# Kernel tuning notes

Measured on AMD Instinct MI355X. Metric: run time of the kernel, lower is better.

## Reference

```python
import jax, jax.numpy as jnp
import numpy as np

H = 8  # num_heads

def setup_inputs() -> dict:
    key = jax.random.key(0)
    ks = jax.random.split(key, 10)
    B, N, D, E = 1, 4096, 256, 65536
    s = 0.02
    return {
        "x": jax.random.normal(ks[0], (B, N, D), jnp.float32),
        "edge_index": jax.random.randint(ks[1], (2, E), 0, N, jnp.int32),
        "edge_attr": jax.random.normal(ks[2], (E, 3), jnp.float32),
        "Wq": jax.random.normal(ks[3], (D, D), jnp.float32) * s,
        "bq": jnp.zeros((D,), jnp.float32),
        "Wk": jax.random.normal(ks[4], (D, D), jnp.float32) * s,
        "bk": jnp.zeros((D,), jnp.float32),
        "Wv": jax.random.normal(ks[5], (D, D), jnp.float32) * s,
        "bv": jnp.zeros((D,), jnp.float32),
        "Wo": jax.random.normal(ks[6], (D, D), jnp.float32) * s,
        "bo": jnp.zeros((D,), jnp.float32),
        "We": jax.random.normal(ks[7], (3, H), jnp.float32) * s,
        "be": jnp.zeros((H,), jnp.float32),
    }

def reference(x, edge_index, edge_attr, Wq, bq, Wk, bk, Wv, bv, Wo, bo, We, be):
    B, N, D = x.shape
    hd = D // H
    q = (x @ Wq + bq).reshape(B, N, H, hd)
    k = (x @ Wk + bk).reshape(B, N, H, hd)
    v = (x @ Wv + bv).reshape(B, N, H, hd)
    # scores: [B, H, N, N]
    scores = jnp.einsum("bihd,bjhd->bhij", q, k) / jnp.sqrt(jnp.asarray(hd, x.dtype))
    # edge bias: torch scatter_ writes a row-constant value into column edge_tgt
    # for every query row (edge_src unused in the original). Equivalent to a
    # per-head column bias [H, N], broadcast over batch and query rows.
    eb = edge_attr @ We + be            # [E, H]
    edge_tgt = edge_index[1]
    col_bias = jnp.zeros((H, N), x.dtype).at[:, edge_tgt].set(eb.T)  # [H, N]
    scores = scores + col_bias[None, :, None, :]
    attn = jax.nn.softmax(scores, axis=-1)
    out = jnp.einsum("bhij,bjhd->bihd", attn, v).reshape(B, N, D)
    return out @ Wo + bo
```

## Files before the change

### kernel.cpp

```cpp
#include <hip/hip_runtime.h>
#include <hip/hip_bf16.h>
#include <math.h>

#define NUM_H 8
#define HD 32
#define DD 256
#define NSPLIT 2
#define KVBLK 64

typedef __attribute__((ext_vector_type(8))) short bf16x8;
typedef __attribute__((ext_vector_type(4))) float f32x4;

__device__ __forceinline__ unsigned short f2b(float f) {
  unsigned u = __builtin_bit_cast(unsigned, f);
  u += 0x7FFFu + ((u >> 16) & 1u);
  return (unsigned short)(u >> 16);
}

__device__ __forceinline__ unsigned pack2(float a, float b) {
  float2 t; t.x = a; t.y = b;
  __hip_bfloat162 r = __float22bfloat162_rn(t);
  unsigned u;
  __builtin_memcpy(&u, &r, sizeof(u));
  return u;
}

#define LOG2E 1.4426950408889634f


__global__ void sel_scatter_kernel(const int* __restrict__ tgt, int* __restrict__ sel, int E) {
  int e = blockIdx.x * 256 + threadIdx.x;
  if (e < E) atomicMax(&sel[tgt[e]], e);
}

__global__ void cvt_all(const float* __restrict__ W0, const float* __restrict__ W1,
                        const float* __restrict__ W2, const float* __restrict__ W3,
                        unsigned short* __restrict__ T0, unsigned short* __restrict__ T1,
                        unsigned short* __restrict__ T2, unsigned short* __restrict__ T3,
                        const float* __restrict__ x, unsigned short* __restrict__ xf,
                        int* __restrict__ sel, int N) {
  const int z = blockIdx.z;
  const int tid = threadIdx.x;
  if (z == 5) {
    const int b = blockIdx.x * 8 + blockIdx.y;
    if (b < (N + 255) / 256) {
      int t = b * 256 + tid;
      if (t < N) sel[t] = -1;
    }
    return;
  }
  if (z == 4) {
    const int b = blockIdx.x * 8 + blockIdx.y;
    const int ntiles = N / 16;
    for (int tt = 0; tt < ntiles / 64; ++tt) {
      const int t4 = b * (ntiles / 64) + tt;
#pragma unroll
      for (int gi = 0; gi < 2; ++gi) {
        const int g = tid + gi * 256;
        const int lr = g >> 5, kk = (g >> 2) & 7, lg = g & 3;
        const float* src = x + ((size_t)t4 * 16 + lr) * DD + kk * 32 + lg * 8;
        const float4 a = *reinterpret_cast<const float4*>(src);
        const float4 c = *reinterpret_cast<const float4*>(src + 4);
        uint4 o;
        o.x = pack2(a.x, a.y); o.y = pack2(a.z, a.w);
        o.z = pack2(c.x, c.y); o.w = pack2(c.z, c.w);
        *reinterpret_cast<uint4*>(xf + (size_t)t4 * 4096 + kk * 512 + lg * 128 + lr * 8) = o;
      }
    }
    return;
  }
  __shared__ float t[32][33];
  const float* W = (z == 0) ? W0 : (z == 1) ? W1 : (z == 2) ? W2 : W3;
  unsigned short* WF = (z == 0) ? T0 : (z == 1) ? T1 : (z == 2) ? T2 : T3;
  const int bx = blockIdx.x, by = blockIdx.y;
  const int lx = tid & 31, ly = tid >> 5;
#pragma unroll
  for (int r = 0; r < 32; r += 8)
    t[r + ly][lx] = W[(size_t)(bx * 32 + r + ly) * DD + by * 32 + lx];
  __syncthreads();
  if (tid < 128) {
    const int ct = tid & 31, lg = tid >> 5;
    bf16x8 val;
#pragma unroll
    for (int e = 0; e < 8; ++e)
      val[e] = (short)f2b(t[lg * 8 + e][ct]);
    const int off = (by * 8 + bx) * 1024 + (ct >> 4) * 512 + lg * 128 + (ct & 15) * 8;
    *reinterpret_cast<bf16x8*>(WF + off) = val;
  }
}

__global__ __launch_bounds__(256) void proj_qkv(const unsigned short* __restrict__ Xf,
                                                const unsigned short* __restrict__ WTq,
                                                const unsigned short* __restrict__ WTk,
                                                const unsigned short* __restrict__ WTv,
                                                const float* __restrict__ bq,
                                                const float* __restrict__ bk,
                                                const float* __restrict__ bv,
                                                unsigned short* __restrict__ qfrag,
                                                unsigned short* __restrict__ kfrag,
                                                unsigned short* __restrict__ vfrag,
                                                const int* __restrict__ sel,
                                                const float* __restrict__ ea,
                                                const float* __restrict__ We,
                                                const float* __restrict__ be,
                                                float* __restrict__ biasg, int N) {
  const int z = blockIdx.z;
  const int tid = threadIdx.x;
  if (z == 3) {
    const int b = blockIdx.x * 8 + blockIdx.y;
    if (b >= (N + 255) / 256) return;
    const int t = b * 256 + tid;
    if (t >= N) return;
    int e = sel[t];
    bool has = (e >= 0);
    float a0 = 0.f, a1 = 0.f, a2 = 0.f;
    if (has) {
      a0 = ea[3 * (size_t)e];
      a1 = ea[3 * (size_t)e + 1];
      a2 = ea[3 * (size_t)e + 2];
    }
#pragma unroll
    for (int h = 0; h < NUM_H; ++h) {
      float v = has ? (a0 * We[h] + a1 * We[NUM_H + h] + a2 * We[2 * NUM_H + h] + be[h]) : 0.f;
      biasg[(size_t)h * N + t] = v * LOG2E;
    }
    return;
  }
  const unsigned short* WT = (z == 0) ? WTq : (z == 1) ? WTk : WTv;
  const float* bias = (z == 0) ? bq : (z == 1) ? bk : bv;
  const int w = tid >> 6, l = tid & 63;
  const int lr = l & 15, lg = l >> 4;
  const int nt = blockIdx.x * 4 + w;
  const int n0 = nt * 16;
  const int cb = blockIdx.y;
  const int c0 = cb * 32;
  const int NT = N / 16;
  const f32x4 zero4 = {0.f, 0.f, 0.f, 0.f};
  f32x4 acc0 = zero4, acc1 = zero4;
  const unsigned short* ap = Xf + (size_t)nt * 4096 + lg * 128 + lr * 8;
  const unsigned short* bp = WT + (size_t)cb * 8192 + lg * 128 + lr * 8;
  if (z < 2) {
#pragma unroll
    for (int kk = 0; kk < 8; ++kk) {
      bf16x8 a  = *reinterpret_cast<const bf16x8*>(ap + kk * 512);
      bf16x8 b0 = *reinterpret_cast<const bf16x8*>(bp + kk * 1024);
      bf16x8 b1 = *reinterpret_cast<const bf16x8*>(bp + kk * 1024 + 512);
      acc0 = __builtin_amdgcn_mfma_f32_16x16x32_bf16(b0, a, acc0, 0, 0, 0);
      acc1 = __builtin_amdgcn_mfma_f32_16x16x32_bf16(b1, a, acc1, 0, 0, 0);
    }
    const f32x4 bv0 = *reinterpret_cast<const f32x4*>(bias + c0 + lg * 4);
    const f32x4 bv1 = *reinterpret_cast<const f32x4*>(bias + c0 + 16 + lg * 4);
    unsigned short* QK = z ? kfrag : qfrag;
    const size_t base = ((size_t)cb * NT + nt) * 512;
    const int kf0 = (lg >> 1) * 128, ke = (lg & 1) * 4;
    uint2 o0, o1;
    o0.x = pack2(acc0[0] + bv0[0], acc0[1] + bv0[1]);
    o0.y = pack2(acc0[2] + bv0[2], acc0[3] + bv0[3]);
    o1.x = pack2(acc1[0] + bv1[0], acc1[1] + bv1[1]);
    o1.y = pack2(acc1[2] + bv1[2], acc1[3] + bv1[3]);
    *reinterpret_cast<uint2*>(QK + base + kf0 + lr * 8 + ke) = o0;
    *reinterpret_cast<uint2*>(QK + base + 256 + kf0 + lr * 8 + ke) = o1;
  } else {
#pragma unroll
    for (int kk = 0; kk < 8; ++kk) {
      bf16x8 a  = *reinterpret_cast<const bf16x8*>(ap + kk * 512);
      bf16x8 b0 = *reinterpret_cast<const bf16x8*>(bp + kk * 1024);
      bf16x8 b1 = *reinterpret_cast<const bf16x8*>(bp + kk * 1024 + 512);
      acc0 = __builtin_amdgcn_mfma_f32_16x16x32_bf16(a, b0, acc0, 0, 0, 0);
      acc1 = __builtin_amdgcn_mfma_f32_16x16x32_bf16(a, b1, acc1, 0, 0, 0);
    }
    const float bc0 = bias[c0 + lr], bc1 = bias[c0 + 16 + lr];
    const int lgf = ((n0 & 16) >> 3) + (lg >> 1);
    const int ke = (lg & 1) * 4;
    const size_t vbase = ((size_t)cb * (N / 32) + (n0 >> 5)) * 1024;
    uint2 o0, o1;
    o0.x = pack2(acc0[0] + bc0, acc0[1] + bc0);
    o0.y = pack2(acc0[2] + bc0, acc0[3] + bc0);
    o1.x = pack2(acc1[0] + bc1, acc1[1] + bc1);
    o1.y = pack2(acc1[2] + bc1, acc1[3] + bc1);
    *reinterpret_cast<uint2*>(vfrag + vbase + lgf * 128 + lr * 8 + ke) = o0;
    *reinterpret_cast<uint2*>(vfrag + vbase + 512 + lgf * 128 + lr * 8 + ke) = o1;
  }
}

__global__ __launch_bounds__(256) void proj_out(const unsigned short* __restrict__ Obf,
                                                const unsigned short* __restrict__ WT,
                                                const float* __restrict__ bias,
                                                float* __restrict__ Y, int N) {
  const int w = threadIdx.x >> 6, l = threadIdx.x & 63;
  const int lr = l & 15, lg = l >> 4;
  const int nt = blockIdx.x * 4 + w;
  const int n0 = nt * 16;
  const int cb = blockIdx.y;
  const int c0 = cb * 32;
  const f32x4 zero4 = {0.f, 0.f, 0.f, 0.f};
  f32x4 acc0 = zero4, acc1 = zero4;
  const unsigned short* ap = Obf + (size_t)nt * 4096 + lg * 128 + lr * 8;
  const unsigned short* bp = WT + (size_t)cb * 8192 + lg * 128 + lr * 8;
#pragma unroll
  for (int kk = 0; kk < 8; ++kk) {
    bf16x8 a  = *reinterpret_cast<const bf16x8*>(ap + kk * 512);
    bf16x8 b0 = *reinterpret_cast<const bf16x8*>(bp + kk * 1024);
    bf16x8 b1 = *reinterpret_cast<const bf16x8*>(bp + kk * 1024 + 512);
    acc0 = __builtin_amdgcn_mfma_f32_16x16x32_bf16(a, b0, acc0, 0, 0, 0);
    acc1 = __builtin_amdgcn_mfma_f32_16x16x32_bf16(a, b1, acc1, 0, 0, 0);
  }
  const float bc0 = bias[c0 + lr], bc1 = bias[c0 + 16 + lr];
#pragma unroll
  for (int r = 0; r < 4; ++r) {
    Y[(size_t)(n0 + lg * 4 + r) * DD + c0 + lr]      = acc0[r] + bc0;
    Y[(size_t)(n0 + lg * 4 + r) * DD + c0 + 16 + lr] = acc1[r] + bc1;
  }
}

__global__ __launch_bounds__(256, 5) void attn_mfma(const unsigned short* __restrict__ qfrag,
                                                    const unsigned short* __restrict__ kfrag,
                                                    const unsigned short* __restrict__ vfrag,
                                                    const float* __restrict__ biasg,
                                                    float* __restrict__ Opart,
                                                    float* __restrict__ lpart, int N) {
  __shared__ unsigned short KVs[2 * 4096];
  __shared__ unsigned short P_lds[4][16 * 64];
  __shared__ float Bs[2048];
  const int tid = threadIdx.x;
  const int w = tid >> 6, l = tid & 63;
  const int lr = l & 15, lg = l >> 4;
  const int bid = blockIdx.x;
  const int h = bid & 7;
  const int rem = bid >> 3;
  const int qblk = rem & 63;
  const int s = rem >> 6;
  const int q0 = qblk * 64 + w * 16;
  const int NT = N / 16;
  const int jlo = s * (N / NSPLIT), jhi = jlo + N / NSPLIT;
  const float scl2 = 0.17677669529663687f * LOG2E;

  const bf16x8 qf = *reinterpret_cast<const bf16x8*>(
      qfrag + ((size_t)h * NT + (q0 >> 4)) * 512 + l * 8);

#pragma unroll
  for (int i = 0; i < 2; ++i)
    *reinterpret_cast<float4*>(&Bs[tid * 4 + i * 1024]) =
        *reinterpret_cast<const float4*>(biasg + (size_t)h * N + jlo + tid * 4 + i * 1024);

  unsigned short* Prow = P_lds[w] + lr * 64;
  const int swz = lr & 7;

  float lsum = 0.f;
  const f32x4 zero4 = {0.f, 0.f, 0.f, 0.f};
  f32x4 oacc0 = zero4, oacc1 = zero4;

  size_t koff = ((size_t)h * NT + (jlo >> 4)) * 512 + tid * 8;
  size_t voff = ((size_t)h * (N / 32) + (jlo >> 5)) * 1024 + tid * 8;
  bf16x8 kreg = *reinterpret_cast<const bf16x8*>(kfrag + koff);
  bf16x8 vreg = *reinterpret_cast<const bf16x8*>(vfrag + voff);

  int buf = 0;
  for (int j0 = jlo; j0 < jhi; j0 += KVBLK) {
    *reinterpret_cast<bf16x8*>(&KVs[buf * 4096 + tid * 8]) = kreg;
    *reinterpret_cast<bf16x8*>(&KVs[buf * 4096 + 2048 + tid * 8]) = vreg;
    if (j0 + KVBLK < jhi) {
      kreg = *reinterpret_cast<const bf16x8*>(kfrag + koff + 2048);
      vreg = *reinterpret_cast<const bf16x8*>(vfrag + voff + 2048);
      koff += 2048; voff += 2048;
    }
    asm volatile("s_waitcnt lgkmcnt(0)" ::: "memory");
    __builtin_amdgcn_s_barrier();
    __builtin_amdgcn_sched_barrier(0);

    const unsigned short* Kb = &KVs[buf * 4096];
    const unsigned short* Vb = &KVs[buf * 4096 + 2048];

    f32x4 sc[4];
    __builtin_amdgcn_s_setprio(1);
#pragma unroll
    for (int jf = 0; jf < 4; ++jf) {
      const bf16x8 kf = *reinterpret_cast<const bf16x8*>(Kb + jf * 512 + l * 8);
      sc[jf] = __builtin_amdgcn_mfma_f32_16x16x32_bf16(kf, qf, zero4, 0, 0, 0);
    }
    __builtin_amdgcn_s_setprio(0);

    float rsum = 0.f;
#pragma unroll
    for (int jf = 0; jf < 4; ++jf) {
      const f32x4 b4 = *reinterpret_cast<const f32x4*>(&Bs[(j0 - jlo) + jf * 16 + lg * 4]);
      float e0 = __builtin_amdgcn_exp2f(sc[jf][0] * scl2 + b4[0]);
      float e1 = __builtin_amdgcn_exp2f(sc[jf][1] * scl2 + b4[1]);
      float e2 = __builtin_amdgcn_exp2f(sc[jf][2] * scl2 + b4[2]);
      float e3 = __builtin_amdgcn_exp2f(sc[jf][3] * scl2 + b4[3]);
      rsum += (e0 + e1) + (e2 + e3);
      uint2 pk;
      pk.x = pack2(e0, e1);
      pk.y = pack2(e2, e3);
      *reinterpret_cast<uint2*>(Prow + (((2 * jf + (lg >> 1)) ^ swz) << 3) + (lg & 1) * 4) = pk;
    }
    rsum += __shfl_xor(rsum, 16);
    rsum += __shfl_xor(rsum, 32);
    lsum += rsum;

    __builtin_amdgcn_s_setprio(1);
#pragma unroll
    for (int c = 0; c < 2; ++c) {
      const bf16x8 pf = *reinterpret_cast<const bf16x8*>(Prow + (((c * 4 + lg) ^ swz) << 3));
      const bf16x8 v0 = *reinterpret_cast<const bf16x8*>(Vb + (c * 2 + 0) * 512 + l * 8);
      const bf16x8 v1 = *reinterpret_cast<const bf16x8*>(Vb + (c * 2 + 1) * 512 + l * 8);
      oacc0 = __builtin_amdgcn_mfma_f32_16x16x32_bf16(pf, v0, oacc0, 0, 0, 0);
      oacc1 = __builtin_amdgcn_mfma_f32_16x16x32_bf16(pf, v1, oacc1, 0, 0, 0);
    }
    __builtin_amdgcn_s_setprio(0);

    buf ^= 1;
  }

  const size_t srow = ((size_t)s * NUM_H + h) * N;
  if (lg == 0) lpart[srow + q0 + lr] = lsum;
  float* Ob = Opart + (srow + q0) * 32;
#pragma unroll
  for (int r = 0; r < 4; ++r) {
    Ob[(size_t)(lg * 4 + r) * 32 + lr]      = oacc0[r];
    Ob[(size_t)(lg * 4 + r) * 32 + 16 + lr] = oacc1[r];
  }
}

__global__ __launch_bounds__(256) void combine_kernel(const float* __restrict__ Op,
                                                      const float* __restrict__ lp,
                                                      unsigned short* __restrict__ obf, int N) {
  const int idx = blockIdx.x * 256 + threadIdx.x;
  const int d4 = idx & 7;
  const int row = idx >> 3;
  const size_t HN = (size_t)NUM_H * N;
  float wsum = 0.f;
#pragma unroll
  for (int s = 0; s < NSPLIT; ++s) wsum += lp[s * HN + row];
  const float inv = 1.f / wsum;
  float4 acc = make_float4(0.f, 0.f, 0.f, 0.f);
#pragma unroll
  for (int s = 0; s < NSPLIT; ++s) {
    const float4 v = *reinterpret_cast<const float4*>(Op + (s * HN + row) * 32 + d4 * 4);
    acc.x += v.x; acc.y += v.y; acc.z += v.z; acc.w += v.w;
  }
  const int h = row / N, n = row - h * N;
  uint2 o;
  o.x = pack2(acc.x * inv, acc.y * inv);
  o.y = pack2(acc.z * inv, acc.w * inv);
  const int off = (n >> 4) * 4096 + h * 512 + (d4 >> 1) * 128 + (n & 15) * 8 + (d4 & 1) * 4;
  *reinterpret_cast<uint2*>(obf + off) = o;
}

extern "C" void kernel_launch(void* const* d_in, const int* in_sizes, int n_in,
                              void* d_out, int out_size, void* d_ws, size_t ws_size,
                              hipStream_t stream) {
  const float* x  = (const float*)d_in[0];
  const int* eidx = (const int*)d_in[1];
  const float* ea = (const float*)d_in[2];
  const float* Wq = (const float*)d_in[3];
  const float* bq = (const float*)d_in[4];
  const float* Wk = (const float*)d_in[5];
  const float* bk = (const float*)d_in[6];
  const float* Wv = (const float*)d_in[7];
  const float* bv = (const float*)d_in[8];
  const float* Wo = (const float*)d_in[9];
  const float* bo = (const float*)d_in[10];
  const float* We = (const float*)d_in[11];
  const float* be = (const float*)d_in[12];
  float* out = (float*)d_out;

  const int N = in_sizes[0] / DD;
  const int E = in_sizes[1] / 2;
  const int* tgt = eidx + E;

  unsigned short* xf    = (unsigned short*)d_ws;
  unsigned short* qfrag = xf    + (size_t)N * DD;
  unsigned short* kfrag = qfrag + (size_t)N * DD;
  unsigned short* vfrag = kfrag + (size_t)N * DD;
  unsigned short* obf   = vfrag + (size_t)N * DD;
  unsigned short* WTq   = obf   + (size_t)N * DD;
  unsigned short* WTk = WTq + DD * DD;
  unsigned short* WTv = WTk + DD * DD;
  unsigned short* WTo = WTv + DD * DD;
  float* bias  = (float*)(WTo + DD * DD);
  float* Opart = bias + (size_t)NUM_H * N;
  float* lpart = Opart + (size_t)NSPLIT * NUM_H * N * 32;
  int*   sel   = (int*)(lpart + (size_t)NSPLIT * NUM_H * N);

  dim3 cg(8, 8, 6);
  cvt_all<<<cg, 256, 0, stream>>>(Wq, Wk, Wv, Wo, WTq, WTk, WTv, WTo, x, xf, sel, N);

  sel_scatter_kernel<<<(E + 255) / 256, 256, 0, stream>>>(tgt, sel, E);

  dim3 pg(N / 64, DD / 32, 4);
  proj_qkv<<<pg, 256, 0, stream>>>(xf, WTq, WTk, WTv, bq, bk, bv, qfrag, kfrag, vfrag,
                                   sel, ea, We, be, bias, N);

  attn_mfma<<<(N / 64) * NUM_H * NSPLIT, 256, 0, stream>>>(qfrag, kfrag, vfrag, bias,
                                                           Opart, lpart, N);

  combine_kernel<<<(NUM_H * N * 8) / 256, 256, 0, stream>>>(Opart, lpart, obf, N);

  dim3 og(N / 64, DD / 32);
  proj_out<<<og, 256, 0, stream>>>(obf, WTo, bo, out, N);
}
```

Before: 75.52 us.

## Permute K fragment layout so softmax P stays in registers, drop LDS staging

The projection kernel now writes K rows in a permuted order, so the score MFMA output layout directly matches the A-operand layout of the PV MFMA. P no longer needs an LDS round trip, and the bias reads are remapped to match. The attention loop also stops staging K/V through shared memory with barriers: each wave loads K/V fragments straight from global memory into registers, double-buffered across tiles. The cost is more register pressure (occupancy hint lowered from 5 to 4) and redundant global/L2 reads of K/V across the four waves.

```diff
diff --git a/kernel.cpp b/kernel.cpp
--- a/kernel.cpp
+++ b/kernel.cpp
@@ -151,15 +151,26 @@
     const f32x4 bv0 = *reinterpret_cast<const f32x4*>(bias + c0 + lg * 4);
     const f32x4 bv1 = *reinterpret_cast<const f32x4*>(bias + c0 + 16 + lg * 4);
     unsigned short* QK = z ? kfrag : qfrag;
-    const size_t base = ((size_t)cb * NT + nt) * 512;
+    size_t base;
+    int rowoff;
+    if (z == 1) {
+      const int j = ((nt & 3) << 4) + lr;
+      const int pos = ((j >> 5) * 2 + ((j >> 2) & 1)) * 16 + (((j & 31) >> 3) << 2) + (j & 3);
+      const int t16p = ((nt >> 2) << 2) + (pos >> 4);
+      base = ((size_t)cb * NT + t16p) * 512;
+      rowoff = (pos & 15) * 8;
+    } else {
+      base = ((size_t)cb * NT + nt) * 512;
+      rowoff = lr * 8;
+    }
     const int kf0 = (lg >> 1) * 128, ke = (lg & 1) * 4;
     uint2 o0, o1;
     o0.x = pack2(acc0[0] + bv0[0], acc0[1] + bv0[1]);
     o0.y = pack2(acc0[2] + bv0[2], acc0[3] + bv0[3]);
     o1.x = pack2(acc1[0] + bv1[0], acc1[1] + bv1[1]);
     o1.y = pack2(acc1[2] + bv1[2], acc1[3] + bv1[3]);
-    *reinterpret_cast<uint2*>(QK + base + kf0 + lr * 8 + ke) = o0;
-    *reinterpret_cast<uint2*>(QK + base + 256 + kf0 + lr * 8 + ke) = o1;
+    *reinterpret_cast<uint2*>(QK + base + kf0 + rowoff + ke) = o0;
+    *reinterpret_cast<uint2*>(QK + base + 256 + kf0 + rowoff + ke) = o1;
   } else {
 #pragma unroll
     for (int kk = 0; kk < 8; ++kk) {
@@ -213,14 +224,52 @@
   }
 }
 
-__global__ __launch_bounds__(256, 5) void attn_mfma(const unsigned short* __restrict__ qfrag,
+__device__ __forceinline__ void attn_tile(const bf16x8 qf, const bf16x8* kf, const bf16x8* vf,
+                                          const float* __restrict__ Bs, int tbase, int lg,
+                                          float scl2, float& lsum, f32x4& oacc0, f32x4& oacc1) {
+  const f32x4 zero4 = {0.f, 0.f, 0.f, 0.f};
+  f32x4 sc[4];
+  __builtin_amdgcn_s_setprio(1);
+#pragma unroll
+  for (int jf = 0; jf < 4; ++jf)
+    sc[jf] = __builtin_amdgcn_mfma_f32_16x16x32_bf16(kf[jf], qf, zero4, 0, 0, 0);
+  __builtin_amdgcn_s_setprio(0);
+
+  float rsum = 0.f;
+  unsigned pk[8];
+#pragma unroll
+  for (int jf = 0; jf < 4; ++jf) {
+    const f32x4 b4 = *reinterpret_cast<const f32x4*>(
+        &Bs[tbase + (jf >> 1) * 32 + lg * 8 + (jf & 1) * 4]);
+    float e0 = __builtin_amdgcn_exp2f(sc[jf][0] * scl2 + b4[0]);
+    float e1 = __builtin_amdgcn_exp2f(sc[jf][1] * scl2 + b4[1]);
+    float e2 = __builtin_amdgcn_exp2f(sc[jf][2] * scl2 + b4[2]);
+    float e3 = __builtin_amdgcn_exp2f(sc[jf][3] * scl2 + b4[3]);
+    rsum += (e0 + e1) + (e2 + e3);
+    pk[jf * 2]     = pack2(e0, e1);
+    pk[jf * 2 + 1] = pack2(e2, e3);
+  }
+  rsum += __shfl_xor(rsum, 16);
+  rsum += __shfl_xor(rsum, 32);
+  lsum += rsum;
+
+  bf16x8 pfA, pfB;
+  __builtin_memcpy(&pfA, &pk[0], 16);
+  __builtin_memcpy(&pfB, &pk[4], 16);
+  __builtin_amdgcn_s_setprio(1);
+  oacc0 = __builtin_amdgcn_mfma_f32_16x16x32_bf16(pfA, vf[0], oacc0, 0, 0, 0);
+  oacc1 = __builtin_amdgcn_mfma_f32_16x16x32_bf16(pfA, vf[1], oacc1, 0, 0, 0);
+  oacc0 = __builtin_amdgcn_mfma_f32_16x16x32_bf16(pfB, vf[2], oacc0, 0, 0, 0);
+  oacc1 = __builtin_amdgcn_mfma_f32_16x16x32_bf16(pfB, vf[3], oacc1, 0, 0, 0);
+  __builtin_amdgcn_s_setprio(0);
+}
+
+__global__ __launch_bounds__(256, 4) void attn_mfma(const unsigned short* __restrict__ qfrag,
                                                     const unsigned short* __restrict__ kfrag,
                                                     const unsigned short* __restrict__ vfrag,
                                                     const float* __restrict__ biasg,
                                                     float* __restrict__ Opart,
                                                     float* __restrict__ lpart, int N) {
-  __shared__ unsigned short KVs[2 * 4096];
-  __shared__ unsigned short P_lds[4][16 * 64];
   __shared__ float Bs[2048];
   const int tid = threadIdx.x;
   const int w = tid >> 6, l = tid & 63;
@@ -232,7 +281,7 @@
   const int s = rem >> 6;
   const int q0 = qblk * 64 + w * 16;
   const int NT = N / 16;
-  const int jlo = s * (N / NSPLIT), jhi = jlo + N / NSPLIT;
+  const int jlo = s * (N / NSPLIT);
   const float scl2 = 0.17677669529663687f * LOG2E;
 
   const bf16x8 qf = *reinterpret_cast<const bf16x8*>(
@@ -242,75 +291,43 @@
   for (int i = 0; i < 2; ++i)
     *reinterpret_cast<float4*>(&Bs[tid * 4 + i * 1024]) =
         *reinterpret_cast<const float4*>(biasg + (size_t)h * N + jlo + tid * 4 + i * 1024);
-
-  unsigned short* Prow = P_lds[w] + lr * 64;
-  const int swz = lr & 7;
+  __syncthreads();
+
+  const unsigned short* kb_ = kfrag + ((size_t)h * NT + (jlo >> 4)) * 512 + l * 8;
+  const unsigned short* vb_ = vfrag + ((size_t)h * (N / 32) + (jlo >> 5)) * 1024 + l * 8;
 
   float lsum = 0.f;
   const f32x4 zero4 = {0.f, 0.f, 0.f, 0.f};
   f32x4 oacc0 = zero4, oacc1 = zero4;
 
-  size_t koff = ((size_t)h * NT + (jlo >> 4)) * 512 + tid * 8;
-  size_t voff = ((size_t)h * (N / 32) + (jlo >> 5)) * 1024 + tid * 8;
-  bf16x8 kreg = *reinterpret_cast<const bf16x8*>(kfrag + koff);
-  bf16x8 vreg = *reinterpret_cast<const bf16x8*>(vfrag + voff);
-
-  int buf = 0;
-  for (int j0 = jlo; j0 < jhi; j0 += KVBLK) {
-    *reinterpret_cast<bf16x8*>(&KVs[buf * 4096 + tid * 8]) = kreg;
-    *reinterpret_cast<bf16x8*>(&KVs[buf * 4096 + 2048 + tid * 8]) = vreg;
-    if (j0 + KVBLK < jhi) {
-      kreg = *reinterpret_cast<const bf16x8*>(kfrag + koff + 2048);
-      vreg = *reinterpret_cast<const bf16x8*>(vfrag + voff + 2048);
-      koff += 2048; voff += 2048;
-    }
-    asm volatile("s_waitcnt lgkmcnt(0)" ::: "memory");
-    __builtin_amdgcn_s_barrier();
-    __builtin_amdgcn_sched_barrier(0);
-
-    const unsigned short* Kb = &KVs[buf * 4096];
-    const unsigned short* Vb = &KVs[buf * 4096 + 2048];
-
-    f32x4 sc[4];
-    __builtin_amdgcn_s_setprio(1);
-#pragma unroll
-    for (int jf = 0; jf < 4; ++jf) {
-      const bf16x8 kf = *reinterpret_cast<const bf16x8*>(Kb + jf * 512 + l * 8);
-      sc[jf] = __builtin_amdgcn_mfma_f32_16x16x32_bf16(kf, qf, zero4, 0, 0, 0);
-    }
-    __builtin_amdgcn_s_setprio(0);
-
-    float rsum = 0.f;
-#pragma unroll
-    for (int jf = 0; jf < 4; ++jf) {
-      const f32x4 b4 = *reinterpret_cast<const f32x4*>(&Bs[(j0 - jlo) + jf * 16 + lg * 4]);
-      float e0 = __builtin_amdgcn_exp2f(sc[jf][0] * scl2 + b4[0]);
-      float e1 = __builtin_amdgcn_exp2f(sc[jf][1] * scl2 + b4[1]);
-      float e2 = __builtin_amdgcn_exp2f(sc[jf][2] * scl2 + b4[2]);
-      float e3 = __builtin_amdgcn_exp2f(sc[jf][3] * scl2 + b4[3]);
-      rsum += (e0 + e1) + (e2 + e3);
-      uint2 pk;
-      pk.x = pack2(e0, e1);
-      pk.y = pack2(e2, e3);
-      *reinterpret_cast<uint2*>(Prow + (((2 * jf + (lg >> 1)) ^ swz) << 3) + (lg & 1) * 4) = pk;
-    }
-    rsum += __shfl_xor(rsum, 16);
-    rsum += __shfl_xor(rsum, 32);
-    lsum += rsum;
-
-    __builtin_amdgcn_s_setprio(1);
-#pragma unroll
-    for (int c = 0; c < 2; ++c) {
-      const bf16x8 pf = *reinterpret_cast<const bf16x8*>(Prow + (((c * 4 + lg) ^ swz) << 3));
-      const bf16x8 v0 = *reinterpret_cast<const bf16x8*>(Vb + (c * 2 + 0) * 512 + l * 8);
-      const bf16x8 v1 = *reinterpret_cast<const bf16x8*>(Vb + (c * 2 + 1) * 512 + l * 8);
-      oacc0 = __builtin_amdgcn_mfma_f32_16x16x32_bf16(pf, v0, oacc0, 0, 0, 0);
-      oacc1 = __builtin_amdgcn_mfma_f32_16x16x32_bf16(pf, v1, oacc1, 0, 0, 0);
-    }
-    __builtin_amdgcn_s_setprio(0);
-
-    buf ^= 1;
-  }
+#define LOADK(dst, t)                                                               \
+  {                                                                                 \
+    _Pragma("unroll") for (int jf = 0; jf < 4; ++jf)                                \
+        dst[jf] = *reinterpret_cast<const bf16x8*>(kb_ + ((t) * 4 + jf) * 512);     \
+  }
+#define LOADV(dst, t)                                                               \
+  {                                                                                 \
+    _Pragma("unroll") for (int cd = 0; cd < 4; ++cd)                                \
+        dst[cd] = *reinterpret_cast<const bf16x8*>(vb_ + ((t) * 2 + (cd >> 1)) * 1024 \
+                                                   + (cd & 1) * 512);               \
+  }
+
+  const int ntiles = (N / NSPLIT) >> 6;
+  bf16x8 kA[4], vA[4], kB[4], vB[4];
+  LOADK(kA, 0);
+  LOADV(vA, 0);
+  for (int t = 0; t < ntiles; t += 2) {
+    LOADK(kB, t + 1);
+    LOADV(vB, t + 1);
+    attn_tile(qf, kA, vA, Bs, t * 64, lg, scl2, lsum, oacc0, oacc1);
+    if (t + 2 < ntiles) {
+      LOADK(kA, t + 2);
+      LOADV(vA, t + 2);
+    }
+    attn_tile(qf, kB, vB, Bs, (t + 1) * 64, lg, scl2, lsum, oacc0, oacc1);
+  }
+#undef LOADK
+#undef LOADV
 
   const size_t srow = ((size_t)s * NUM_H + h) * N;
   if (lg == 0) lpart[srow + q0 + lr] = lsum;
```

New measurement: 70.26 us. 1.07x faster.
